# Kernel tuning notes

Measured on AMD Instinct MI355X. Metric: run time of the kernel, lower is better.

The kernel has to match this reference:

```python
import jax, jax.numpy as jnp
import numpy as np

N, L, HH, WW, E, NH = 8, 300, 96, 96, 256, 8


def setup_inputs() -> dict:
    key = jax.random.key(0)
    ks = jax.random.split(key, 9)
    return {
        "query_row": jax.random.normal(ks[0], (N, L, E), dtype=jnp.float32),
        "query_col": jax.random.normal(ks[1], (N, L, E), dtype=jnp.float32),
        "key_row": jax.random.normal(ks[2], (N, HH, WW, E), dtype=jnp.float32),
        "key_col": jax.random.normal(ks[3], (N, HH, WW, E), dtype=jnp.float32),
        "value": jax.random.normal(ks[4], (N, HH, WW, E), dtype=jnp.float32),
        "in_proj_weight": jax.random.normal(ks[5], (5 * E, E), dtype=jnp.float32) * 0.02,
        "in_proj_bias": jax.random.normal(ks[6], (5 * E,), dtype=jnp.float32) * 0.02,
        "out_proj_weight": jax.random.normal(ks[7], (E, E), dtype=jnp.float32) * 0.02,
        "out_proj_bias": jax.random.normal(ks[8], (E,), dtype=jnp.float32) * 0.02,
        "num_heads": NH,
    }


def reference(query_row, query_col, key_row, key_col, value,
              in_proj_weight, in_proj_bias, out_proj_weight, out_proj_bias,
              num_heads):
    bsz, tgt_len, embed_dim = query_row.shape
    head_dim = embed_dim // num_heads
    scaling = float(head_dim) ** -0.5

    def proj(x, i):
        w = in_proj_weight[i * embed_dim:(i + 1) * embed_dim]
        b = in_proj_bias[i * embed_dim:(i + 1) * embed_dim]
        return x @ w.T + b

    q_row = proj(query_row, 0) * scaling          # (N, L, E)
    q_col = proj(query_col, 1) * scaling          # (N, L, E)
    k_row = proj(key_row, 2).mean(axis=1)         # mean over H -> (N, W, E)
    k_col = proj(key_col, 3).mean(axis=2)         # mean over W -> (N, H, E)
    v = proj(value, 4)                            # (N, H, W, E)

    heads = lambda t: t.reshape(*t.shape[:-1], num_heads, head_dim)
    qr, qc, kr, kc = heads(q_row), heads(q_col), heads(k_row), heads(k_col)
    vh = heads(v)                                 # (N, H, W, nh, hd)

    # additive row/col decomposed scores -> independent softmaxes
    w_row = jax.nn.softmax(jnp.einsum('blnd,bwnd->bnlw', qr, kr), axis=-1)  # (N,nh,L,W)
    w_col = jax.nn.softmax(jnp.einsum('blnd,bhnd->bnlh', qc, kc), axis=-1)  # (N,nh,L,H)

    # contract col weights with value over H, then row weights over W
    tmp = jnp.einsum('bnlh,bhwnd->bnlwd', w_col, vh)       # (N,nh,L,W,hd)
    out = jnp.einsum('bnlw,bnlwd->blnd', w_row, tmp)       # (N,L,nh,hd)
    out = out.reshape(bsz, tgt_len, embed_dim).transpose(1, 0, 2)  # (L,N,E)
    return out @ out_proj_weight.T + out_proj_bias
```

## Files before the change

kernel.cpp:

```cpp
#include <hip/hip_runtime.h>
#include <cstdint>


typedef __attribute__((ext_vector_type(8))) short short8v;
typedef __attribute__((ext_vector_type(4))) short short4v;
typedef __attribute__((ext_vector_type(4))) float f32x4;

#define SCALE_Q 0.17677669529663687f

#define GLL16(gp, lp)                                                   \
  __builtin_amdgcn_global_load_lds(                                     \
      (const __attribute__((address_space(1))) void*)(gp),              \
      (__attribute__((address_space(3))) void*)(lp), 16, 0, 0)

__device__ __forceinline__ unsigned short f2bf(float x) {
  unsigned int u = __builtin_bit_cast(unsigned int, x);
  u += 0x7FFFu + ((u >> 16) & 1u);
  return (unsigned short)(u >> 16);
}

__device__ __forceinline__ unsigned int cvtpk(float a, float b) {
  unsigned int r;
  asm("v_cvt_pk_bf16_f32 %0, %1, %2" : "=v"(r) : "v"(a), "v"(b));
  return r;
}

__device__ __forceinline__ short8v pack8cvt(const f32x4& lo, const f32x4& hi) {
  union { short8v s; unsigned int u[4]; } z;
  z.u[0] = cvtpk(lo[0], lo[1]);
  z.u[1] = cvtpk(lo[2], lo[3]);
  z.u[2] = cvtpk(hi[0], hi[1]);
  z.u[3] = cvtpk(hi[2], hi[3]);
  return z.s;
}

__device__ __forceinline__ short4v pack4cvt(float a, float b, float c, float d) {
  union { short4v s; unsigned int u[2]; } z;
  z.u[0] = cvtpk(a, b);
  z.u[1] = cvtpk(c, d);
  return z.s;
}

__device__ __forceinline__ short8v pack8(const float4& fa, const float4& fb) {
  short8v v;
  v[0] = (short)f2bf(fa.x); v[1] = (short)f2bf(fa.y);
  v[2] = (short)f2bf(fa.z); v[3] = (short)f2bf(fa.w);
  v[4] = (short)f2bf(fb.x); v[5] = (short)f2bf(fb.y);
  v[6] = (short)f2bf(fb.z); v[7] = (short)f2bf(fb.w);
  return v;
}

__global__ __launch_bounds__(256) void cvt_w_kernel(const float* __restrict__ w_in,
                                                    const float* __restrict__ w_out,
                                                    short* __restrict__ Wb) {
  int idx = blockIdx.x * 256 + threadIdx.x;
  float v = (idx < 327680) ? w_in[idx] : w_out[idx - 327680];
  Wb[idx] = (short)f2bf(v);
}

__global__ __launch_bounds__(256) void mean_over_h_v3(const float* __restrict__ in,
                                                      float* __restrict__ out) {
  __shared__ float4 part[256];
  int bw = blockIdx.x;
  int b = bw / 96, w = bw - b * 96;
  int t = threadIdx.x, e4 = t & 63, hq = t >> 6;
  const float4* p = (const float4*)(in + ((size_t)b * 9216 + w) * 256) + e4 +
                    (size_t)hq * 24 * 6144;
  float4 s = {0.f, 0.f, 0.f, 0.f};
#pragma unroll
  for (int i = 0; i < 24; ++i) {
    float4 v = p[(size_t)i * 6144];
    s.x += v.x; s.y += v.y; s.z += v.z; s.w += v.w;
  }
  part[t] = s;
  __syncthreads();
  if (t < 64) {
    float4 a = part[t], c = part[t + 64], d = part[t + 128], e = part[t + 192];
    float4 o;
    o.x = (a.x + c.x + d.x + e.x) * (1.f / 96.f);
    o.y = (a.y + c.y + d.y + e.y) * (1.f / 96.f);
    o.z = (a.z + c.z + d.z + e.z) * (1.f / 96.f);
    o.w = (a.w + c.w + d.w + e.w) * (1.f / 96.f);
    ((float4*)out)[(size_t)bw * 64 + t] = o;
  }
}

__global__ __launch_bounds__(256) void mean_over_w_v3(const float* __restrict__ in,
                                                      float* __restrict__ out) {
  __shared__ float4 part[256];
  int bh = blockIdx.x;
  int t = threadIdx.x, e4 = t & 63, wq = t >> 6;
  const float4* p = (const float4*)(in + (size_t)bh * 24576) + e4 + (size_t)wq * 24 * 64;
  float4 s = {0.f, 0.f, 0.f, 0.f};
#pragma unroll
  for (int i = 0; i < 24; ++i) {
    float4 v = p[(size_t)i * 64];
    s.x += v.x; s.y += v.y; s.z += v.z; s.w += v.w;
  }
  part[t] = s;
  __syncthreads();
  if (t < 64) {
    float4 a = part[t], c = part[t + 64], d = part[t + 128], e = part[t + 192];
    float4 o;
    o.x = (a.x + c.x + d.x + e.x) * (1.f / 96.f);
    o.y = (a.y + c.y + d.y + e.y) * (1.f / 96.f);
    o.z = (a.z + c.z + d.z + e.z) * (1.f / 96.f);
    o.w = (a.w + c.w + d.w + e.w) * (1.f / 96.f);
    ((float4*)out)[(size_t)bh * 64 + t] = o;
  }
}

__global__ __launch_bounds__(256) void gemm_proj(
    const float* __restrict__ A0, const float* __restrict__ A1,
    const short* __restrict__ Wb, const float* __restrict__ bias,
    float* __restrict__ Cf, short* __restrict__ Cb0, short* __restrict__ Cb1,
    float scale, int mode) {
  __shared__ short As[32 * 264];
  int y = blockIdx.y;
  const float* A = y ? A1 : A0;
  short* Cb = y ? Cb1 : Cb0;
  const short* Wp = Wb + y * 65536;
  const float* bp = bias + y * 256;
  int t = threadIdx.x;
  int m0 = blockIdx.x * 32;
  int wave = t >> 6, lane = t & 63, r = lane & 15, g = lane >> 4;

  {
    int row = t >> 3, c0 = (t & 7) * 32;
    const float* ap = A + ((size_t)m0 + row) * 256 + c0;
    float4 ld[8];
#pragma unroll
    for (int j = 0; j < 8; ++j) ld[j] = *(const float4*)(ap + j * 4);
    short* dst = &As[row * 264 + c0];
#pragma unroll
    for (int j = 0; j < 4; ++j)
      *(short8v*)(dst + j * 8) = pack8(ld[2 * j], ld[2 * j + 1]);
  }
  __syncthreads();

  f32x4 acc[2][4] = {};
  const short* wbase = Wp + (size_t)(wave * 64 + r) * 256;
#pragma unroll
  for (int ks = 0; ks < 8; ++ks) {
    short8v af0 = *(const short8v*)&As[r * 264 + ks * 32 + g * 8];
    short8v af1 = *(const short8v*)&As[(16 + r) * 264 + ks * 32 + g * 8];
    short8v bf[4];
#pragma unroll
    for (int nf = 0; nf < 4; ++nf)
      bf[nf] = *(const short8v*)(wbase + nf * 16 * 256 + ks * 32 + g * 8);
#pragma unroll
    for (int nf = 0; nf < 4; ++nf) {
      acc[0][nf] = __builtin_amdgcn_mfma_f32_16x16x32_bf16(af0, bf[nf], acc[0][nf], 0, 0, 0);
      acc[1][nf] = __builtin_amdgcn_mfma_f32_16x16x32_bf16(af1, bf[nf], acc[1][nf], 0, 0, 0);
    }
  }

#pragma unroll
  for (int mf = 0; mf < 2; ++mf)
#pragma unroll
    for (int nf = 0; nf < 4; ++nf) {
      int nn = wave * 64 + nf * 16 + r;
      float bval = bp[nn];
#pragma unroll
      for (int i = 0; i < 4; ++i) {
        int m = m0 + mf * 16 + g * 4 + i;
        float val = (acc[mf][nf][i] + bval) * scale;
        if (mode == 1) {
          int bb = m / 300, ll = m - bb * 300;
          Cf[((size_t)ll * 8 + bb) * 256 + nn] = val;
        } else {
          Cb[(size_t)m * 256 + nn] = (short)f2bf(val);
        }
      }
    }
}

__global__ __launch_bounds__(256, 2) void vproj_kernel(
    const float* __restrict__ A, const short* __restrict__ Wb,
    const float* __restrict__ bias, short* __restrict__ vvT) {
  __shared__ float buf[2][16 * 260];
  __shared__ short Ts[4][64 * 68];
  int t = threadIdx.x;
  int wave = t >> 6, lane = t & 63, r = lane & 15, g = lane >> 4;
  int m0g = blockIdx.x * 288;
  int b_ = blockIdx.x >> 5;
  int hw00 = (blockIdx.x & 31) * 288;

  short8v bf[8][4];
  {
    const short* wbase = Wb + (size_t)(wave * 64 + r) * 256;
#pragma unroll
    for (int ks = 0; ks < 8; ++ks)
#pragma unroll
      for (int nf = 0; nf < 4; ++nf)
        bf[ks][nf] = *(const short8v*)(wbase + nf * 16 * 256 + ks * 32 + g * 8);
  }
#pragma unroll
  for (int ks = 0; ks < 8; ++ks)
#pragma unroll
    for (int nf = 0; nf < 4; ++nf)
      asm volatile("" : "+a"(bf[ks][nf]));
  float bias_v[4];
#pragma unroll
  for (int nf = 0; nf < 4; ++nf) bias_v[nf] = bias[wave * 64 + nf * 16 + r];

#pragma unroll
  for (int q = 0; q < 2; ++q) {
#pragma unroll
    for (int i = 0; i < 4; ++i) {
      int row = wave * 4 + i;
      const float* gp = A + ((size_t)m0g + q * 16 + row) * 256 + lane * 4;
      GLL16(gp, &buf[q][row * 260]);
    }
  }

  int chg = wave * 64 + lane;
  short* vbase = vvT + (size_t)(b_ * 8 + (chg >> 5)) * 294912 +
                 (size_t)(chg & 31) * 9216 + hw00;
  const short* tsr = &Ts[wave][lane * 68];

#pragma unroll
  for (int tt = 0; tt < 18; ++tt) {
    if (tt == 17)                    asm volatile("s_waitcnt vmcnt(0)" ::: "memory");
    else if ((tt & 3) == 0 && tt)    asm volatile("s_waitcnt vmcnt(12)" ::: "memory");
    else                             asm volatile("s_waitcnt vmcnt(4)" ::: "memory");
    __builtin_amdgcn_s_barrier();

    f32x4 acc[4] = {};
    const float* bp_ = &buf[tt & 1][0];
#pragma unroll
    for (int ks = 0; ks < 8; ++ks) {
      const float* p = bp_ + r * 260 + ks * 32 + g * 8;
      f32x4 lo = *(const f32x4*)p;
      f32x4 hi = *(const f32x4*)(p + 4);
      short8v af = pack8cvt(lo, hi);
#pragma unroll
      for (int nf = 0; nf < 4; ++nf)
        acc[nf] = __builtin_amdgcn_mfma_f32_16x16x32_bf16(af, bf[ks][nf], acc[nf], 0, 0, 0);
    }

#pragma unroll
    for (int nf = 0; nf < 4; ++nf) {
      float bv = bias_v[nf];
      *(short4v*)&Ts[wave][(nf * 16 + r) * 68 + (tt & 3) * 16 + g * 4] =
          pack4cvt(acc[nf][0] + bv, acc[nf][1] + bv, acc[nf][2] + bv, acc[nf][3] + bv);
    }
    asm volatile("" ::: "memory");

    if ((tt & 3) == 3) {
      short* gdst = vbase + (tt >> 2) * 64;
#pragma unroll
      for (int j = 0; j < 8; ++j)
        *(short8v*)(gdst + j * 8) = *(const short8v*)(tsr + j * 8);
      asm volatile("" ::: "memory");
    } else if (tt == 17) {
      short* gdst = vbase + 256;
#pragma unroll
      for (int j = 0; j < 4; ++j)
        *(short8v*)(gdst + j * 8) = *(const short8v*)(tsr + j * 8);
      asm volatile("" ::: "memory");
    }

    __builtin_amdgcn_s_barrier();
    if (tt + 2 < 18) {
#pragma unroll
      for (int i = 0; i < 4; ++i) {
        int row = wave * 4 + i;
        const float* gp = A + ((size_t)m0g + (tt + 2) * 16 + row) * 256 + lane * 4;
        GLL16(gp, &buf[tt & 1][row * 260]);
      }
    }
  }
}

__global__ __launch_bounds__(64) void scores_softmax_v2(
    const short* __restrict__ qrb, const short* __restrict__ qcb,
    const short* __restrict__ krb, const short* __restrict__ kcb,
    short* __restrict__ wrowB, float* __restrict__ wcolT) {
  int lchunk = blockIdx.x, bn = blockIdx.y, kind = blockIdx.z;
  int b = bn >> 3, n = bn & 7;
  int lane = threadIdx.x;
  int r = lane & 15, g = lane >> 4;
  const short* qb = kind ? qcb : qrb;
  const short* kb = kind ? kcb : krb;
  int l0 = lchunk * 80;

  short8v a[5], bfr[6];
#pragma unroll
  for (int lf = 0; lf < 5; ++lf) {
    int l = l0 + lf * 16 + r;
    if (l > 299) l = 299;
    a[lf] = *(const short8v*)(qb + ((size_t)b * 300 + l) * 256 + n * 32 + g * 8);
  }
#pragma unroll
  for (int f = 0; f < 6; ++f)
    bfr[f] = *(const short8v*)(kb + ((size_t)b * 96 + f * 16 + r) * 256 + n * 32 + g * 8);

  f32x4 c[5][6];
#pragma unroll
  for (int lf = 0; lf < 5; ++lf)
#pragma unroll
    for (int f = 0; f < 6; ++f) {
      f32x4 z = {};
      c[lf][f] = __builtin_amdgcn_mfma_f32_16x16x32_bf16(a[lf], bfr[f], z, 0, 0, 0);
    }

#pragma unroll
  for (int lf = 0; lf < 5; ++lf)
#pragma unroll
    for (int i = 0; i < 4; ++i) {
      float m = c[lf][0][i];
#pragma unroll
      for (int f = 1; f < 6; ++f) m = fmaxf(m, c[lf][f][i]);
#pragma unroll
      for (int mask = 1; mask <= 8; mask <<= 1) m = fmaxf(m, __shfl_xor(m, mask, 64));
      float e[6], s = 0.f;
#pragma unroll
      for (int f = 0; f < 6; ++f) { e[f] = __expf(c[lf][f][i] - m); s += e[f]; }
#pragma unroll
      for (int mask = 1; mask <= 8; mask <<= 1) s += __shfl_xor(s, mask, 64);
      float inv = 1.f / s;
#pragma unroll
      for (int f = 0; f < 6; ++f) c[lf][f][i] = e[f] * inv;
    }

  if (kind == 0) {
#pragma unroll
    for (int lf = 0; lf < 5; ++lf)
#pragma unroll
      for (int i = 0; i < 4; ++i) {
        int l = l0 + lf * 16 + g * 4 + i;
        bool ok = (l < 300);
#pragma unroll
        for (int f = 0; f < 6; ++f) {
          float wv = ok ? c[lf][f][i] : 0.f;
          wrowB[((size_t)bn * 320 + l) * 96 + f * 16 + r] = (short)f2bf(wv);
        }
      }
  } else {
#pragma unroll
    for (int lf = 0; lf < 5; ++lf)
#pragma unroll
      for (int f = 0; f < 6; ++f) {
        int l = l0 + lf * 16 + g * 4;
        f32x4 wv = c[lf][f];
#pragma unroll
        for (int i = 0; i < 4; ++i) if (l + i >= 300) wv[i] = 0.f;
        *(f32x4*)(wcolT + ((size_t)bn * 96 + f * 16 + r) * 320 + l) = wv;
      }
  }
}

__global__ __launch_bounds__(512) void attn_kernel(
    const short* __restrict__ wrowB, const float* __restrict__ wcolT,
    const short* __restrict__ vvT, float* __restrict__ ao) {
  __shared__ f32x4 cmb[3][2][4][64];
  int lh = blockIdx.x, n = blockIdx.y, b = blockIdx.z;
  int bn = b * 8 + n;
  int t = threadIdx.x, wave = t >> 6, lane = t & 63;
  int df = wave & 1, hh = wave >> 1;
  int lbase = lh * 64;
  int r = lane & 15, g = lane >> 4;

  short8v a[4][3];
  const short* wr = wrowB + (size_t)bn * 320 * 96;
#pragma unroll
  for (int lf = 0; lf < 4; ++lf)
#pragma unroll
    for (int ks = 0; ks < 3; ++ks)
      a[lf][ks] = *(const short8v*)(wr + (lbase + lf * 16 + r) * 96 + ks * 32 + g * 8);

  const short* vb = vvT + (size_t)bn * 294912 + (size_t)(df * 16 + r) * 9216 + hh * 24 * 96;
  const float* wcb = wcolT + ((size_t)bn * 96 + hh * 24) * 320 + lbase + g * 4;

  f32x4 acc[4] = {};
  short8v b0[3], b1[3];
  f32x4 w0[4], w1[4];
#pragma unroll
  for (int ks = 0; ks < 3; ++ks) b0[ks] = *(const short8v*)(vb + ks * 32 + g * 8);
#pragma unroll
  for (int lf = 0; lf < 4; ++lf) w0[lf] = *(const f32x4*)(wcb + lf * 16);

  for (int h2 = 0; h2 < 12; ++h2) {
    int h = h2 * 2;
#pragma unroll
    for (int ks = 0; ks < 3; ++ks) b1[ks] = *(const short8v*)(vb + (h + 1) * 96 + ks * 32 + g * 8);
#pragma unroll
    for (int lf = 0; lf < 4; ++lf) w1[lf] = *(const f32x4*)(wcb + (h + 1) * 320 + lf * 16);
    {
      f32x4 R[4] = {};
#pragma unroll
      for (int ks = 0; ks < 3; ++ks)
#pragma unroll
        for (int lf = 0; lf < 4; ++lf)
          R[lf] = __builtin_amdgcn_mfma_f32_16x16x32_bf16(a[lf][ks], b0[ks], R[lf], 0, 0, 0);
#pragma unroll
      for (int lf = 0; lf < 4; ++lf) acc[lf] += w0[lf] * R[lf];
    }
    if (h2 < 11) {
#pragma unroll
      for (int ks = 0; ks < 3; ++ks) b0[ks] = *(const short8v*)(vb + (h + 2) * 96 + ks * 32 + g * 8);
#pragma unroll
      for (int lf = 0; lf < 4; ++lf) w0[lf] = *(const f32x4*)(wcb + (h + 2) * 320 + lf * 16);
    }
    {
      f32x4 R[4] = {};
#pragma unroll
      for (int ks = 0; ks < 3; ++ks)
#pragma unroll
        for (int lf = 0; lf < 4; ++lf)
          R[lf] = __builtin_amdgcn_mfma_f32_16x16x32_bf16(a[lf][ks], b1[ks], R[lf], 0, 0, 0);
#pragma unroll
      for (int lf = 0; lf < 4; ++lf) acc[lf] += w1[lf] * R[lf];
    }
  }

  if (hh > 0) {
#pragma unroll
    for (int lf = 0; lf < 4; ++lf) cmb[hh - 1][df][lf][lane] = acc[lf];
  }
  __syncthreads();
  if (hh == 0) {
#pragma unroll
    for (int lf = 0; lf < 4; ++lf) {
      f32x4 o = acc[lf];
#pragma unroll
      for (int q = 0; q < 3; ++q) o += cmb[q][df][lf][lane];
#pragma unroll
      for (int i = 0; i < 4; ++i) {
        int l = lbase + lf * 16 + g * 4 + i;
        if (l < 300)
          ao[((size_t)b * 300 + l) * 256 + n * 32 + df * 16 + r] = o[i];
      }
    }
  }
}

extern "C" void kernel_launch(void* const* d_in, const int* in_sizes, int n_in,
                              void* d_out, int out_size, void* d_ws, size_t ws_size,
                              hipStream_t stream) {
  const float* query_row = (const float*)d_in[0];
  const float* query_col = (const float*)d_in[1];
  const float* key_row   = (const float*)d_in[2];
  const float* key_col   = (const float*)d_in[3];
  const float* value     = (const float*)d_in[4];
  const float* W         = (const float*)d_in[5];
  const float* Bv        = (const float*)d_in[6];
  const float* Wout      = (const float*)d_in[7];
  const float* Bout      = (const float*)d_in[8];

  float* ws = (float*)d_ws;
  float* krm   = ws;
  float* kcm   = krm + 196608;
  float* ao    = kcm + 196608;
  float* wcolT = ao + 614400;
  short* qrb   = (short*)(wcolT + 1966080);
  short* qcb   = qrb + 614400;
  short* krb   = qcb + 614400;
  short* kcb   = krb + 196608;
  short* wrowB = kcb + 196608;
  short* vvT   = wrowB + 1966080;
  short* Wb    = vvT + 18874368;

  cvt_w_kernel<<<1536, 256, 0, stream>>>(W, Wout, Wb);
  mean_over_h_v3<<<768, 256, 0, stream>>>(key_row, krm);
  mean_over_w_v3<<<768, 256, 0, stream>>>(key_col, kcm);
  gemm_proj<<<dim3(75, 2), 256, 0, stream>>>(query_row, query_col, Wb, Bv,
                                             nullptr, qrb, qcb, SCALE_Q, 3);
  gemm_proj<<<dim3(24, 2), 256, 0, stream>>>(krm, kcm, Wb + 131072, Bv + 512,
                                             nullptr, krb, kcb, 1.f, 3);
  vproj_kernel<<<256, 256, 0, stream>>>(value, Wb + 262144, Bv + 1024, vvT);
  scores_softmax_v2<<<dim3(4, 64, 2), 64, 0, stream>>>(qrb, qcb, krb, kcb, wrowB, wcolT);
  attn_kernel<<<dim3(5, 8, 8), 512, 0, stream>>>(wrowB, wcolT, vvT, ao);
  gemm_proj<<<dim3(75, 1), 256, 0, stream>>>(ao, nullptr, Wb + 327680, Bout,
                                             (float*)d_out, nullptr, nullptr, 1.f, 1);
}
```

Baseline: 160.5 us.

## Widen vproj to 8 waves and remap attn blocks for XCD locality

The value-projection kernel now runs 512 threads per block, so each wave covers 32 output channels instead of 64. This halves per-wave B-fragment registers and the load/store work per wave while keeping the same tile per block, with the vmcnt wait counts adjusted to match. The attention kernel moves to a flat 320-block grid whose index is decoded so that all L-chunks of a given (batch, head) land on the same XCD, improving L2 reuse of that head's value and weight data. The risk is lower occupancy for vproj (one block per CU) and more barrier participants per block.

Measured after the change: 159.6 us. About the same (-0.6%).

```diff
diff --git a/kernel.cpp b/kernel.cpp
--- a/kernel.cpp
+++ b/kernel.cpp
@@ -175,58 +175,60 @@
     }
 }
 
-__global__ __launch_bounds__(256, 2) void vproj_kernel(
+__global__ __launch_bounds__(512, 1) void vproj_kernel(
     const float* __restrict__ A, const short* __restrict__ Wb,
     const float* __restrict__ bias, short* __restrict__ vvT) {
   __shared__ float buf[2][16 * 260];
-  __shared__ short Ts[4][64 * 68];
+  __shared__ short Ts[8][32 * 68];
   int t = threadIdx.x;
   int wave = t >> 6, lane = t & 63, r = lane & 15, g = lane >> 4;
   int m0g = blockIdx.x * 288;
   int b_ = blockIdx.x >> 5;
   int hw00 = (blockIdx.x & 31) * 288;
-
-  short8v bf[8][4];
+  int chbase = wave * 32;
+
+  short8v bf[8][2];
   {
-    const short* wbase = Wb + (size_t)(wave * 64 + r) * 256;
+    const short* wbase = Wb + (size_t)(chbase + r) * 256;
 #pragma unroll
     for (int ks = 0; ks < 8; ++ks)
 #pragma unroll
-      for (int nf = 0; nf < 4; ++nf)
+      for (int nf = 0; nf < 2; ++nf)
         bf[ks][nf] = *(const short8v*)(wbase + nf * 16 * 256 + ks * 32 + g * 8);
   }
 #pragma unroll
   for (int ks = 0; ks < 8; ++ks)
 #pragma unroll
-    for (int nf = 0; nf < 4; ++nf)
+    for (int nf = 0; nf < 2; ++nf)
       asm volatile("" : "+a"(bf[ks][nf]));
-  float bias_v[4];
-#pragma unroll
-  for (int nf = 0; nf < 4; ++nf) bias_v[nf] = bias[wave * 64 + nf * 16 + r];
+  float bias_v[2];
+#pragma unroll
+  for (int nf = 0; nf < 2; ++nf) bias_v[nf] = bias[chbase + nf * 16 + r];
 
 #pragma unroll
   for (int q = 0; q < 2; ++q) {
 #pragma unroll
-    for (int i = 0; i < 4; ++i) {
-      int row = wave * 4 + i;
+    for (int i = 0; i < 2; ++i) {
+      int row = wave * 2 + i;
       const float* gp = A + ((size_t)m0g + q * 16 + row) * 256 + lane * 4;
       GLL16(gp, &buf[q][row * 260]);
     }
   }
 
-  int chg = wave * 64 + lane;
+  int chg = chbase + (lane & 31);
+  int half = lane >> 5;
   short* vbase = vvT + (size_t)(b_ * 8 + (chg >> 5)) * 294912 +
                  (size_t)(chg & 31) * 9216 + hw00;
-  const short* tsr = &Ts[wave][lane * 68];
+  const short* tsr = &Ts[wave][(lane & 31) * 68];
 
 #pragma unroll
   for (int tt = 0; tt < 18; ++tt) {
-    if (tt == 17)                    asm volatile("s_waitcnt vmcnt(0)" ::: "memory");
-    else if ((tt & 3) == 0 && tt)    asm volatile("s_waitcnt vmcnt(12)" ::: "memory");
-    else                             asm volatile("s_waitcnt vmcnt(4)" ::: "memory");
+    if (tt == 17)                 asm volatile("s_waitcnt vmcnt(0)" ::: "memory");
+    else if (tt && (tt & 3) == 0) asm volatile("s_waitcnt vmcnt(6)" ::: "memory");
+    else                          asm volatile("s_waitcnt vmcnt(2)" ::: "memory");
     __builtin_amdgcn_s_barrier();
 
-    f32x4 acc[4] = {};
+    f32x4 acc[2] = {};
     const float* bp_ = &buf[tt & 1][0];
 #pragma unroll
     for (int ks = 0; ks < 8; ++ks) {
@@ -234,13 +236,12 @@
       f32x4 lo = *(const f32x4*)p;
       f32x4 hi = *(const f32x4*)(p + 4);
       short8v af = pack8cvt(lo, hi);
-#pragma unroll
-      for (int nf = 0; nf < 4; ++nf)
-        acc[nf] = __builtin_amdgcn_mfma_f32_16x16x32_bf16(af, bf[ks][nf], acc[nf], 0, 0, 0);
-    }
-
-#pragma unroll
-    for (int nf = 0; nf < 4; ++nf) {
+      acc[0] = __builtin_amdgcn_mfma_f32_16x16x32_bf16(af, bf[ks][0], acc[0], 0, 0, 0);
+      acc[1] = __builtin_amdgcn_mfma_f32_16x16x32_bf16(af, bf[ks][1], acc[1], 0, 0, 0);
+    }
+
+#pragma unroll
+    for (int nf = 0; nf < 2; ++nf) {
       float bv = bias_v[nf];
       *(short4v*)&Ts[wave][(nf * 16 + r) * 68 + (tt & 3) * 16 + g * 4] =
           pack4cvt(acc[nf][0] + bv, acc[nf][1] + bv, acc[nf][2] + bv, acc[nf][3] + bv);
@@ -248,24 +249,26 @@
     asm volatile("" ::: "memory");
 
     if ((tt & 3) == 3) {
-      short* gdst = vbase + (tt >> 2) * 64;
-#pragma unroll
-      for (int j = 0; j < 8; ++j)
-        *(short8v*)(gdst + j * 8) = *(const short8v*)(tsr + j * 8);
+      short* gdst = vbase + (tt >> 2) * 64 + half * 32;
+      const short* src = tsr + half * 32;
+#pragma unroll
+      for (int j = 0; j < 4; ++j)
+        *(short8v*)(gdst + j * 8) = *(const short8v*)(src + j * 8);
       asm volatile("" ::: "memory");
     } else if (tt == 17) {
-      short* gdst = vbase + 256;
-#pragma unroll
-      for (int j = 0; j < 4; ++j)
-        *(short8v*)(gdst + j * 8) = *(const short8v*)(tsr + j * 8);
+      short* gdst = vbase + 256 + half * 16;
+      const short* src = tsr + half * 16;
+#pragma unroll
+      for (int j = 0; j < 2; ++j)
+        *(short8v*)(gdst + j * 8) = *(const short8v*)(src + j * 8);
       asm volatile("" ::: "memory");
     }
 
     __builtin_amdgcn_s_barrier();
     if (tt + 2 < 18) {
 #pragma unroll
-      for (int i = 0; i < 4; ++i) {
-        int row = wave * 4 + i;
+      for (int i = 0; i < 2; ++i) {
+        int row = wave * 2 + i;
         const float* gp = A + ((size_t)m0g + (tt + 2) * 16 + row) * 256 + lane * 4;
         GLL16(gp, &buf[tt & 1][row * 260]);
       }
@@ -355,8 +358,11 @@
     const short* __restrict__ wrowB, const float* __restrict__ wcolT,
     const short* __restrict__ vvT, float* __restrict__ ao) {
   __shared__ f32x4 cmb[3][2][4][64];
-  int lh = blockIdx.x, n = blockIdx.y, b = blockIdx.z;
-  int bn = b * 8 + n;
+  int i = blockIdx.x;
+  int xcd = i & 7, j = i >> 3;
+  int bn = (j / 5) * 8 + xcd;
+  int lh = j - (j / 5) * 5;
+  int b = bn >> 3, n = bn & 7;
   int t = threadIdx.x, wave = t >> 6, lane = t & 63;
   int df = wave & 1, hh = wave >> 1;
   int lbase = lh * 64;
@@ -427,10 +433,10 @@
 #pragma unroll
       for (int q = 0; q < 3; ++q) o += cmb[q][df][lf][lane];
 #pragma unroll
-      for (int i = 0; i < 4; ++i) {
-        int l = lbase + lf * 16 + g * 4 + i;
+      for (int i2 = 0; i2 < 4; ++i2) {
+        int l = lbase + lf * 16 + g * 4 + i2;
         if (l < 300)
-          ao[((size_t)b * 300 + l) * 256 + n * 32 + df * 16 + r] = o[i];
+          ao[((size_t)b * 300 + l) * 256 + n * 32 + df * 16 + r] = o[i2];
       }
     }
   }
@@ -469,9 +475,9 @@
                                              nullptr, qrb, qcb, SCALE_Q, 3);
   gemm_proj<<<dim3(24, 2), 256, 0, stream>>>(krm, kcm, Wb + 131072, Bv + 512,
                                              nullptr, krb, kcb, 1.f, 3);
-  vproj_kernel<<<256, 256, 0, stream>>>(value, Wb + 262144, Bv + 1024, vvT);
+  vproj_kernel<<<256, 512, 0, stream>>>(value, Wb + 262144, Bv + 1024, vvT);
   scores_softmax_v2<<<dim3(4, 64, 2), 64, 0, stream>>>(qrb, qcb, krb, kcb, wrowB, wcolT);
-  attn_kernel<<<dim3(5, 8, 8), 512, 0, stream>>>(wrowB, wcolT, vvT, ao);
+  attn_kernel<<<320, 512, 0, stream>>>(wrowB, wcolT, vvT, ao);
   gemm_proj<<<dim3(75, 1), 256, 0, stream>>>(ao, nullptr, Wb + 327680, Bout,
                                              (float*)d_out, nullptr, nullptr, 1.f, 1);
 }
```
